# Performance work log

Measured on AMD Instinct MI355X. Metric: run time of the kernel, lower is better.

Reference implementation:

```python
import jax, jax.numpy as jnp
import numpy as np

N = 4096
FIN = 4096
LOC = 16
H1, H2, HEADS = 120, 50, 4
H1_PER = H1 // HEADS
FILM_Z = 32
SSDB_H = 60
N_HEMI = N // 2
NEG_SLOPE = 0.1
GATE_BIAS = -2.0
MASK_FILL = -9e15


def leaky(x):
    return jax.nn.leaky_relu(x, negative_slope=NEG_SLOPE)


def gat(x, mask, W, a_src, a_dst, bias, concat):
    # x: (N, Fin), W: (H, Fin, O), a_src/a_dst: (H, O), mask: (N, N) bool
    wh = jnp.einsum('nf,hfo->hno', x, W)            # (H, N, O)
    f1 = jnp.einsum('hno,ho->hn', wh, a_src)        # (H, N)
    f2 = jnp.einsum('hno,ho->hn', wh, a_dst)        # (H, N)
    e = leaky(f1[:, :, None] + f2[:, None, :])      # (H, N, N)
    e = jnp.where(mask[None], e, MASK_FILL)
    alpha = jax.nn.softmax(e, axis=-1)
    out = jnp.einsum('hij,hjo->hio', alpha, wh)     # (H, N, O)
    if concat:
        h, n, o = out.shape
        out2 = out.transpose(1, 0, 2).reshape(n, h * o)
    else:
        out2 = out.mean(axis=0)
    return out2 + bias


def _uni(k, shape, stdv):
    return jax.random.uniform(k, shape, jnp.float32, -stdv, stdv)


def setup_inputs() -> dict:
    key = jax.random.key(0)
    ks = jax.random.split(key, 30)
    s1 = 1.0 / np.sqrt(H1_PER)
    s2 = 1.0 / np.sqrt(H2)
    inp = {
        'x_fc': jax.random.normal(ks[0], (N, FIN), jnp.float32),
        'adj': jax.random.randint(ks[1], (N, N), 0, 2, jnp.int32),
        'l_loc': jax.random.uniform(ks[2], (N, LOC), jnp.float32),
        # gat1
        'W1': _uni(ks[3], (HEADS, FIN, H1_PER), s1),
        'a1s': _uni(ks[4], (HEADS, H1_PER), s1),
        'a1d': _uni(ks[5], (HEADS, H1_PER), s1),
        'b1': _uni(ks[6], (H1,), s1),
        # gat2
        'W2': _uni(ks[7], (1, H1, H2), s2),
        'a2s': _uni(ks[8], (1, H2), s2),
        'a2d': _uni(ks[9], (1, H2), s2),
        'b2': _uni(ks[10], (H2,), s2),
        # classifier (no bias)
        'Wc': _uni(ks[11], (2, H2), s2),
        # FiLM trunk
        'Wl1': _uni(ks[12], (FILM_Z, LOC), 1.0 / np.sqrt(LOC)),
        'bl1': _uni(ks[13], (FILM_Z,), 1.0 / np.sqrt(LOC)),
        'Wl2': _uni(ks[14], (FILM_Z, FILM_Z), 1.0 / np.sqrt(FILM_Z)),
        'bl2': _uni(ks[15], (FILM_Z,), 1.0 / np.sqrt(FILM_Z)),
        'Wg': _uni(ks[16], (H2, FILM_Z), 1.0 / np.sqrt(FILM_Z)),
        'bg': _uni(ks[17], (H2,), 1.0 / np.sqrt(FILM_Z)),
        'Wb': _uni(ks[18], (H2, FILM_Z), 1.0 / np.sqrt(FILM_Z)),
        'bb': _uni(ks[19], (H2,), 1.0 / np.sqrt(FILM_Z)),
        'Wgate': _uni(ks[20], (1, FILM_Z), 1.0 / np.sqrt(FILM_Z)),
        'bgate': jnp.full((1,), GATE_BIAS, jnp.float32),
        # SSDB hemi
        'Ws1': _uni(ks[21], (SSDB_H, N_HEMI), 1.0 / np.sqrt(N_HEMI)),
        'bs1': _uni(ks[22], (SSDB_H,), 1.0 / np.sqrt(N_HEMI)),
        'Ws2': _uni(ks[23], (1, SSDB_H), 1.0 / np.sqrt(SSDB_H)),
        'bs2': _uni(ks[24], (1,), 1.0 / np.sqrt(SSDB_H)),
    }
    return inp


def reference(x_fc, adj, l_loc, W1, a1s, a1d, b1, W2, a2s, a2d, b2, Wc,
              Wl1, bl1, Wl2, bl2, Wg, bg, Wb, bb, Wgate, bgate,
              Ws1, bs1, Ws2, bs2):
    mask = adj > 0
    h = leaky(gat(x_fc, mask, W1, a1s, a1d, b1, concat=True))    # (N, 120)
    h = leaky(gat(h, mask, W2, a2s, a2d, b2, concat=False))      # (N, 50)
    # FiLM conditioning
    z = leaky(l_loc @ Wl1.T + bl1)
    z = leaky(z @ Wl2.T + bl2)
    gamma = z @ Wg.T + bg                                        # (N, 50)
    beta = z @ Wb.T + bb                                         # (N, 50)
    g = jax.nn.sigmoid(z @ Wgate.T + bgate)                      # (N, 1)
    cov = jnp.clip(l_loc[:, -1], 0.0, 1.0)                       # coverage_power = 1.0
    g = g * cov[:, None]
    h_fused = h + g * (gamma * h + beta)
    logits = leaky(h_fused @ Wc.T)                               # (N, 2)
    # hemisphere SSDB bias
    t = logits.T                                                 # (2, N)
    ipsi = t[:, :N_HEMI]
    contra = t[:, N_HEMI:2 * N_HEMI]
    h_i = leaky(ipsi @ Ws1.T + bs1)                              # (2, 60)
    h_c = leaky(contra @ Ws1.T + bs1)
    b_i = leaky(h_i @ Ws2.T + bs2)                               # (2, 1)
    b_c = leaky(h_c @ Ws2.T + bs2)
    b_mid = 0.5 * (b_i + b_c)                                    # (2, 1)
    bias_nodes = jnp.concatenate([
        jnp.broadcast_to(b_i.T, (N_HEMI, 2)),
        jnp.broadcast_to(b_c.T, (N_HEMI, 2)),
    ], axis=0)                                                   # n_mid = 0
    logits = logits + bias_nodes
    bias_avg = b_mid[:, 0]                                       # (2,)
    return logits, bias_avg
```

## Files before the change

kernel.cpp:

```cpp
#include <hip/hip_runtime.h>

#define NN 4096
#define HEADS 4
#define H1PER 30
#define H1DIM 120
#define H2DIM 50

typedef short short8_t __attribute__((ext_vector_type(8)));
typedef float f32x4 __attribute__((ext_vector_type(4)));

__device__ __forceinline__ float lrelu(float x) { return x > 0.f ? x : 0.1f * x; }

__device__ __forceinline__ unsigned short bfrne(float x) {
  unsigned u = __float_as_uint(x);
  u += 0x7fffu + ((u >> 16) & 1u);
  return (unsigned short)(u >> 16);
}
__device__ __forceinline__ unsigned bfpk_rne(float lo, float hi) {
  return (unsigned)bfrne(lo) | ((unsigned)bfrne(hi) << 16);
}
__device__ __forceinline__ unsigned bfpk(float lo, float hi) {
  unsigned a = (__float_as_uint(lo) + 0x8000u) >> 16;
  unsigned b = (__float_as_uint(hi) + 0x8000u) & 0xffff0000u;
  return a | b;
}
__device__ __forceinline__ float score(float f2v, float f1r, float mr, unsigned bsel, int jj) {
  float f = f1r + f2v;
  float e = fmaxf(f, 0.1f * f);
  float wv = __expf(e - mr);
  return wv * (float)((bsel >> jj) & 1u);
}

__global__ __launch_bounds__(256) void k_bits(const int* __restrict__ adj,
                                              unsigned long long* __restrict__ bits) {
  size_t base = (size_t)blockIdx.x * 1024;
  int t = threadIdx.x;
  int v0 = adj[base + t];
  int v1 = adj[base + 256 + t];
  int v2 = adj[base + 512 + t];
  int v3 = adj[base + 768 + t];
  unsigned long long m0 = __ballot(v0 > 0);
  unsigned long long m1 = __ballot(v1 > 0);
  unsigned long long m2 = __ballot(v2 > 0);
  unsigned long long m3 = __ballot(v3 > 0);
  if ((t & 63) == 0) {
    size_t w = (base + t) >> 6;
    bits[w] = m0;
    bits[w + 4] = m1;
    bits[w + 8] = m2;
    bits[w + 12] = m3;
  }
}

__global__ __launch_bounds__(256) void k_prep(const float* __restrict__ W1,
                                              const float* __restrict__ a1s,
                                              const float* __restrict__ a1d,
                                              unsigned short* __restrict__ w1t) {
  int k = blockIdx.x * 256 + threadIdx.x;
#pragma unroll
  for (int h = 0; h < 4; ++h) {
    const float* wp = W1 + ((size_t)h * 4096 + k) * H1PER;
    float fs = 0.f, fd = 0.f;
#pragma unroll
    for (int oo = 0; oo < H1PER; ++oo) {
      float v = wp[oo];
      w1t[(size_t)(h * 30 + oo) * 4096 + k] = bfrne(v);
      fs += v * a1s[h * H1PER + oo];
      fd += v * a1d[h * H1PER + oo];
    }
    w1t[(size_t)(120 + h) * 4096 + k] = bfrne(fs);
    w1t[(size_t)(124 + h) * 4096 + k] = bfrne(fd);
  }
}

__global__ __launch_bounds__(256) void k_gemm1s(const float* __restrict__ x,
                                                const unsigned short* __restrict__ w1t,
                                                float* __restrict__ part) {
  const int t = threadIdx.x;
  const int lane = t & 63, wave = t >> 6;
  const int m = lane & 15, q = lane >> 4;
  const int i0 = blockIdx.x * 64;
  const int kz = blockIdx.y * 256;
  const float* xp = x + (size_t)(i0 + wave * 16 + m) * 4096 + kz + q * 8;
  const unsigned short* wb = w1t + (size_t)m * 4096 + kz + q * 8;
  f32x4 acc[8];
#pragma unroll
  for (int nt = 0; nt < 8; ++nt) acc[nt] = (f32x4){0.f, 0.f, 0.f, 0.f};
  float4 a0[2], a1[2];
  short8_t Bv[2][8];
  a0[0] = *(const float4*)(xp);
  a1[0] = *(const float4*)(xp + 4);
#pragma unroll
  for (int nt = 0; nt < 8; ++nt) Bv[0][nt] = *(const short8_t*)(wb + (size_t)nt * 16 * 4096);
#pragma unroll
  for (int ks = 0; ks < 8; ++ks) {
    const int cur = ks & 1, nxt = cur ^ 1;
    if (ks < 7) {
      a0[nxt] = *(const float4*)(xp + (ks + 1) * 32);
      a1[nxt] = *(const float4*)(xp + (ks + 1) * 32 + 4);
#pragma unroll
      for (int nt = 0; nt < 8; ++nt)
        Bv[nxt][nt] = *(const short8_t*)(wb + (ks + 1) * 32 + (size_t)nt * 16 * 4096);
    }
    union { short8_t v; unsigned u[4]; } A;
    A.u[0] = bfpk_rne(a0[cur].x, a0[cur].y);
    A.u[1] = bfpk_rne(a0[cur].z, a0[cur].w);
    A.u[2] = bfpk_rne(a1[cur].x, a1[cur].y);
    A.u[3] = bfpk_rne(a1[cur].z, a1[cur].w);
#pragma unroll
    for (int nt = 0; nt < 8; ++nt)
      acc[nt] = __builtin_amdgcn_mfma_f32_16x16x32_bf16(A.v, Bv[cur][nt], acc[nt], 0, 0, 0);
  }
  float* pp = part + ((size_t)blockIdx.y * 4096 + i0 + wave * 16 + q * 4) * 128 + m;
#pragma unroll
  for (int nt = 0; nt < 8; ++nt)
#pragma unroll
    for (int r = 0; r < 4; ++r) pp[r * 128 + nt * 16] = acc[nt][r];
}

__global__ __launch_bounds__(256) void k_f1c(const float* __restrict__ part,
                                             unsigned short* __restrict__ whbt,
                                             float* __restrict__ f1, float* __restrict__ f2) {
  const int t = threadIdx.x;
  const int n = blockIdx.x * 16 + (t >> 4);
  const int og = (t & 15) * 8;
  float s[8] = {0.f, 0.f, 0.f, 0.f, 0.f, 0.f, 0.f, 0.f};
  for (int z = 0; z < 16; ++z) {
    const float* pp = part + ((size_t)z * NN + n) * 128 + og;
    float4 u0 = *(const float4*)pp;
    float4 u1 = *(const float4*)(pp + 4);
    s[0] += u0.x; s[1] += u0.y; s[2] += u0.z; s[3] += u0.w;
    s[4] += u1.x; s[5] += u1.y; s[6] += u1.z; s[7] += u1.w;
  }
  if (og < 120) {
#pragma unroll
    for (int j = 0; j < 8; ++j) {
      int o = og + j;
      int h = o / 30, oo = o - h * 30;
      whbt[(size_t)(h * 32 + oo) * NN + n] = bfrne(s[j]);
    }
  } else {
#pragma unroll
    for (int j = 0; j < 4; ++j) {
      f1[(size_t)j * NN + n] = s[j];
      f2[(size_t)j * NN + n] = s[4 + j];
    }
  }
  if ((t & 15) < 8) {
    int h = (t & 15) >> 1, odd = (t & 15) & 1;
    whbt[(size_t)(h * 32 + 30 + odd) * NN + n] = odd ? 0 : 0x3f80;
  }
}

__global__ __launch_bounds__(256) void k_max(const float* __restrict__ v, float* __restrict__ mx) {
  int t = threadIdx.x;
  const float* row = v + (size_t)blockIdx.x * NN;
  float m = -3.0e38f;
  for (int n = t; n < NN; n += 256) m = fmaxf(m, row[n]);
  for (int off = 32; off > 0; off >>= 1) m = fmaxf(m, __shfl_down(m, off));
  __shared__ float ms[4];
  if ((t & 63) == 0) ms[t >> 6] = m;
  __syncthreads();
  if (t == 0) mx[blockIdx.x] = fmaxf(fmaxf(ms[0], ms[1]), fmaxf(ms[2], ms[3]));
}

__global__ __launch_bounds__(256) void k_att1m(const unsigned short* __restrict__ whbt,
                                               const float* __restrict__ f1, const float* __restrict__ f2,
                                               const float* __restrict__ mx,
                                               const unsigned int* __restrict__ bits32,
                                               float* __restrict__ part) {
  const int h = blockIdx.y, js = blockIdx.z;
  const int t = threadIdx.x;
  const int lane = t & 63, wave = t >> 6;
  const int m = lane & 15, q = lane >> 4;
  const int i0 = blockIdx.x * 64 + wave * 16;
  const int jbase = js * 2048;
  __shared__ float f2s[2048];
  for (int e = t; e < 2048; e += 256) f2s[e] = f2[h * NN + jbase + e];
  __syncthreads();
  const float f1r = f1[h * NN + i0 + m];
  const float fm = f1r + mx[h];
  const float mr = fmaxf(fm, 0.1f * fm);
  const unsigned int* brow = bits32 + (size_t)(i0 + m) * 128 + (jbase >> 5);
  const unsigned short* bb0 = whbt + (size_t)(h * 32 + m) * NN + jbase + q * 8;
  const unsigned short* bb1 = bb0 + 16 * NN;
  const float* fp = f2s + q * 8;
  f32x4 acc0 = {0.f, 0.f, 0.f, 0.f}, acc1 = {0.f, 0.f, 0.f, 0.f};
  for (int step = 0; step < 64; ++step) {
    const int jl = step * 32;
    unsigned bsel = brow[step] >> (q * 8);
    float4 fa = *(const float4*)(fp + jl);
    float4 fb = *(const float4*)(fp + jl + 4);
    float w0 = score(fa.x, f1r, mr, bsel, 0);
    float w1 = score(fa.y, f1r, mr, bsel, 1);
    float w2 = score(fa.z, f1r, mr, bsel, 2);
    float w3 = score(fa.w, f1r, mr, bsel, 3);
    float w4 = score(fb.x, f1r, mr, bsel, 4);
    float w5 = score(fb.y, f1r, mr, bsel, 5);
    float w6 = score(fb.z, f1r, mr, bsel, 6);
    float w7 = score(fb.w, f1r, mr, bsel, 7);
    union { short8_t v; unsigned u[4]; } A;
    A.u[0] = bfpk(w0, w1);
    A.u[1] = bfpk(w2, w3);
    A.u[2] = bfpk(w4, w5);
    A.u[3] = bfpk(w6, w7);
    short8_t b0 = *(const short8_t*)(bb0 + jl);
    short8_t b1 = *(const short8_t*)(bb1 + jl);
    acc0 = __builtin_amdgcn_mfma_f32_16x16x32_bf16(A.v, b0, acc0, 0, 0, 0);
    acc1 = __builtin_amdgcn_mfma_f32_16x16x32_bf16(A.v, b1, acc1, 0, 0, 0);
  }
  float* pp = part + ((size_t)(js * 4 + h) * NN + i0 + q * 4) * 32 + m;
#pragma unroll
  for (int r = 0; r < 4; ++r) {
    pp[r * 32] = acc0[r];
    pp[r * 32 + 16] = acc1[r];
  }
}

__global__ __launch_bounds__(256) void k_h1(const float* __restrict__ part, const float* __restrict__ b1,
                                            float* __restrict__ h1) {
  int t = threadIdx.x;
  int lane = t & 63;
  int p = lane >> 5, o = lane & 31;
  int id = blockIdx.x * 8 + (t >> 6) * 2 + p;
  int h = id >> 12, n = id & 4095;
  const float* p0 = part + ((size_t)h * NN + n) * 32 + o;
  const float* p1 = part + ((size_t)(4 + h) * NN + n) * 32 + o;
  float tot = p0[0] + p1[0];
  float l = __shfl(tot, p * 32 + 30);
  if (o < H1PER) h1[(size_t)n * H1DIM + h * H1PER + o] = lrelu(tot / l + b1[h * H1PER + o]);
}

__global__ __launch_bounds__(256) void k_gemm2(const float* __restrict__ h1, const float* __restrict__ W2,
                                               float* __restrict__ wh2) {
  const int n0 = blockIdx.x * 4;
  const int t = threadIdx.x;
  const int o = t & 63, r = t >> 6;
  __shared__ float hs[4][120];
  for (int e = t; e < 4 * H1DIM; e += 256) hs[e / H1DIM][e % H1DIM] = h1[(size_t)n0 * H1DIM + e];
  __syncthreads();
  if (o < H2DIM) {
    float acc = 0.f;
#pragma unroll 4
    for (int k = 0; k < H1DIM; ++k) acc += hs[r][k] * W2[k * H2DIM + o];
    wh2[(size_t)(n0 + r) * H2DIM + o] = acc;
  }
}

__global__ __launch_bounds__(256) void k_f2l2(const float* __restrict__ wh2, const float* __restrict__ a2s,
                                              const float* __restrict__ a2d, float* __restrict__ f1,
                                              float* __restrict__ f2, unsigned short* __restrict__ whbt) {
  int n = blockIdx.x * 256 + threadIdx.x;
  if (n >= NN) return;
  const float* r = wh2 + (size_t)n * H2DIM;
  unsigned short* wb = whbt + n;
  float accs = 0.f, accd = 0.f;
#pragma unroll
  for (int j = 0; j < H2DIM; ++j) {
    float v = r[j];
    wb[j * NN] = bfrne(v);
    accs += v * a2s[j];
    accd += v * a2d[j];
  }
  wb[50 * NN] = 0x3f80;
#pragma unroll
  for (int j = 51; j < 64; ++j) wb[j * NN] = 0;
  f1[n] = accs;
  f2[n] = accd;
}

__global__ __launch_bounds__(256) void k_att2m(const unsigned short* __restrict__ whbt,
                                               const float* __restrict__ f1, const float* __restrict__ f2,
                                               const float* __restrict__ mx,
                                               const unsigned int* __restrict__ bits32,
                                               float* __restrict__ part) {
  const int js = blockIdx.y;
  const int t = threadIdx.x;
  const int lane = t & 63, wave = t >> 6;
  const int m = lane & 15, q = lane >> 4;
  const int i0 = blockIdx.x * 64 + wave * 16;
  const int jbase = js * 1024;
  __shared__ float f2s[1024];
  for (int e = t; e < 1024; e += 256) f2s[e] = f2[jbase + e];
  __syncthreads();
  const float f1r = f1[i0 + m];
  const float fm = f1r + mx[0];
  const float mr = fmaxf(fm, 0.1f * fm);
  const unsigned int* brow = bits32 + (size_t)(i0 + m) * 128 + (jbase >> 5);
  const unsigned short* bb = whbt + (size_t)m * NN + jbase + q * 8;
  const float* fp = f2s + q * 8;
  f32x4 acc[4];
#pragma unroll
  for (int x = 0; x < 4; ++x) acc[x] = (f32x4){0.f, 0.f, 0.f, 0.f};
  for (int step = 0; step < 32; ++step) {
    const int jl = step * 32;
    unsigned bsel = brow[step] >> (q * 8);
    float4 fa = *(const float4*)(fp + jl);
    float4 fb = *(const float4*)(fp + jl + 4);
    float w0 = score(fa.x, f1r, mr, bsel, 0);
    float w1 = score(fa.y, f1r, mr, bsel, 1);
    float w2 = score(fa.z, f1r, mr, bsel, 2);
    float w3 = score(fa.w, f1r, mr, bsel, 3);
    float w4 = score(fb.x, f1r, mr, bsel, 4);
    float w5 = score(fb.y, f1r, mr, bsel, 5);
    float w6 = score(fb.z, f1r, mr, bsel, 6);
    float w7 = score(fb.w, f1r, mr, bsel, 7);
    union { short8_t v; unsigned u[4]; } A;
    A.u[0] = bfpk(w0, w1);
    A.u[1] = bfpk(w2, w3);
    A.u[2] = bfpk(w4, w5);
    A.u[3] = bfpk(w6, w7);
#pragma unroll
    for (int tile = 0; tile < 4; ++tile) {
      short8_t b = *(const short8_t*)(bb + (size_t)tile * 16 * NN + jl);
      acc[tile] = __builtin_amdgcn_mfma_f32_16x16x32_bf16(A.v, b, acc[tile], 0, 0, 0);
    }
  }
  float* pp = part + ((size_t)js * NN + i0 + q * 4) * 64 + m;
#pragma unroll
  for (int tile = 0; tile < 4; ++tile)
#pragma unroll
    for (int r = 0; r < 4; ++r) pp[r * 64 + tile * 16] = acc[tile][r];
}

__global__ __launch_bounds__(64) void k_h2(const float* __restrict__ part, const float* __restrict__ b2,
                                           float* __restrict__ h2) {
  int n = blockIdx.x;
  int o = threadIdx.x;
  const float* p = part + (size_t)n * 64 + o;
  float tot = p[0] + p[NN * 64] + p[2 * NN * 64] + p[3 * NN * 64];
  float l = __shfl(tot, 50);
  if (o < H2DIM) h2[(size_t)n * H2DIM + o] = lrelu(tot / l + b2[o]);
}

__global__ __launch_bounds__(256) void k_film(const float* __restrict__ l_loc, const float* __restrict__ h2,
                                              const float* __restrict__ Wl1, const float* __restrict__ bl1,
                                              const float* __restrict__ Wl2, const float* __restrict__ bl2,
                                              const float* __restrict__ Wg, const float* __restrict__ bg,
                                              const float* __restrict__ Wb, const float* __restrict__ bb,
                                              const float* __restrict__ Wgate, const float* __restrict__ bgate,
                                              const float* __restrict__ Wc, float* __restrict__ logits) {
  int n = blockIdx.x * 4 + (threadIdx.x >> 6);
  int lane = threadIdx.x & 63;
  int r32 = lane & 31;
  float locv = l_loc[n * 16 + (lane & 15)];
  float cov = __shfl(locv, 15);
  cov = fminf(fmaxf(cov, 0.f), 1.f);
  float a1v = bl1[r32];
#pragma unroll
  for (int j = 0; j < 16; ++j) a1v += Wl1[r32 * 16 + j] * __shfl(locv, j);
  float z1 = lrelu(a1v);
  float a2v = bl2[r32];
#pragma unroll
  for (int j = 0; j < 32; ++j) a2v += Wl2[r32 * 32 + j] * __shfl(z1, j);
  float z2 = lrelu(a2v);
  float gs = bgate[0];
  float gam, bet;
  {
    int o = lane < H2DIM ? lane : 0;
    gam = bg[o];
    bet = bb[o];
#pragma unroll
    for (int j = 0; j < 32; ++j) {
      float zj = __shfl(z2, j);
      gs += Wgate[j] * zj;
      gam += Wg[o * 32 + j] * zj;
      bet += Wb[o * 32 + j] * zj;
    }
  }
  float g = cov / (1.f + __expf(-gs));
  int o = lane < H2DIM ? lane : 0;
  float hv = h2[(size_t)n * H2DIM + o];
  float hf = hv + g * (gam * hv + bet);
  float p0 = lane < H2DIM ? hf * Wc[o] : 0.f;
  float p1 = lane < H2DIM ? hf * Wc[H2DIM + o] : 0.f;
  for (int off = 32; off > 0; off >>= 1) {
    p0 += __shfl_down(p0, off);
    p1 += __shfl_down(p1, off);
  }
  if (lane == 0) {
    logits[n * 2 + 0] = lrelu(p0);
    logits[n * 2 + 1] = lrelu(p1);
  }
}

__global__ __launch_bounds__(64) void k_ssdb1(const float* __restrict__ logits, const float* __restrict__ Ws1,
                                              float* __restrict__ hsum) {
  int combo = blockIdx.y;
  int hemi = combo >> 1, c = combo & 1;
  int k = threadIdx.x;
  if (k >= 60) return;
  int nbase = blockIdx.x * 256;
  const float* wrow = Ws1 + (size_t)k * 2048 + nbase;
  const float* lcol = logits + (size_t)(hemi * 2048 + nbase) * 2 + c;
  float part = 0.f;
  for (int q = 0; q < 256; ++q) part += wrow[q] * lcol[2 * q];
  atomicAdd(&hsum[combo * 60 + k], part);
}

__global__ __launch_bounds__(256) void k_ssdb2(const float* __restrict__ hsum, const float* __restrict__ bs1,
                                               const float* __restrict__ Ws2, const float* __restrict__ bs2,
                                               float* __restrict__ B) {
  int t = threadIdx.x;
  int combo = t >> 6, k = t & 63;
  float part = 0.f;
  if (k < 60) part = lrelu(hsum[combo * 60 + k] + bs1[k]) * Ws2[k];
  for (int off = 32; off > 0; off >>= 1) part += __shfl_down(part, off);
  if (k == 0) B[combo] = lrelu(part + bs2[0]);
}

__global__ __launch_bounds__(256) void k_final(const float* __restrict__ logits, const float* __restrict__ B,
                                               float* __restrict__ out) {
  int id = blockIdx.x * 256 + threadIdx.x;
  if (id < 2 * NN) {
    int n = id >> 1, c = id & 1;
    out[id] = logits[id] + B[(n < 2048 ? 0 : 2) + c];
  } else if (id < 2 * NN + 2) {
    int c = id - 2 * NN;
    out[id] = 0.5f * (B[c] + B[2 + c]);
  }
}

#define OFF_BITS 0
#define OFF_W1T 524288
#define OFF_GP 786432
#define OFF_A1P 786432
#define OFF_A2P 1835008
#define OFF_H1 2883584
#define OFF_WH2 3375104
#define OFF_WH2BT 3579904
#define OFF_F12 3710976
#define OFF_F22 3715072
#define OFF_MX2 3719168
#define OFF_H2 3719232
#define OFF_LOG 3924032
#define OFF_HSUM 3932224
#define OFF_B 3932480
#define OFF_WH1BT 9175040
#define OFF_F1A 9437184
#define OFF_F2A 9453568
#define OFF_MX1 9469952

extern "C" void kernel_launch(void* const* d_in, const int* in_sizes, int n_in,
                              void* d_out, int out_size, void* d_ws, size_t ws_size,
                              hipStream_t stream) {
  const float* x_fc  = (const float*)d_in[0];
  const int*   adj   = (const int*)d_in[1];
  const float* l_loc = (const float*)d_in[2];
  const float* W1    = (const float*)d_in[3];
  const float* a1s   = (const float*)d_in[4];
  const float* a1d   = (const float*)d_in[5];
  const float* b1    = (const float*)d_in[6];
  const float* W2    = (const float*)d_in[7];
  const float* a2s   = (const float*)d_in[8];
  const float* a2d   = (const float*)d_in[9];
  const float* b2    = (const float*)d_in[10];
  const float* Wc    = (const float*)d_in[11];
  const float* Wl1   = (const float*)d_in[12];
  const float* bl1   = (const float*)d_in[13];
  const float* Wl2   = (const float*)d_in[14];
  const float* bl2   = (const float*)d_in[15];
  const float* Wg    = (const float*)d_in[16];
  const float* bg    = (const float*)d_in[17];
  const float* Wb    = (const float*)d_in[18];
  const float* bb    = (const float*)d_in[19];
  const float* Wgate = (const float*)d_in[20];
  const float* bgate = (const float*)d_in[21];
  const float* Ws1   = (const float*)d_in[22];
  const float* bs1   = (const float*)d_in[23];
  const float* Ws2   = (const float*)d_in[24];
  const float* bs2   = (const float*)d_in[25];
  float* out = (float*)d_out;
  float* w = (float*)d_ws;
  unsigned long long* bits = (unsigned long long*)(w + OFF_BITS);
  const unsigned int* bits32 = (const unsigned int*)bits;
  unsigned short* wh1bt = (unsigned short*)(w + OFF_WH1BT);
  unsigned short* wh2bt = (unsigned short*)(w + OFF_WH2BT);
  unsigned short* w1t = (unsigned short*)(w + OFF_W1T);

  k_bits<<<NN * NN / 1024, 256, 0, stream>>>(adj, bits);
  k_prep<<<16, 256, 0, stream>>>(W1, a1s, a1d, w1t);
  k_gemm1s<<<dim3(64, 16), 256, 0, stream>>>(x_fc, w1t, w + OFF_GP);
  k_f1c<<<256, 256, 0, stream>>>(w + OFF_GP, wh1bt, w + OFF_F1A, w + OFF_F2A);
  k_max<<<HEADS, 256, 0, stream>>>(w + OFF_F2A, w + OFF_MX1);
  k_att1m<<<dim3(64, HEADS, 2), 256, 0, stream>>>(wh1bt, w + OFF_F1A, w + OFF_F2A,
                                                  w + OFF_MX1, bits32, w + OFF_A1P);
  k_h1<<<2048, 256, 0, stream>>>(w + OFF_A1P, b1, w + OFF_H1);
  k_gemm2<<<NN / 4, 256, 0, stream>>>(w + OFF_H1, W2, w + OFF_WH2);
  k_f2l2<<<NN / 256, 256, 0, stream>>>(w + OFF_WH2, a2s, a2d, w + OFF_F12, w + OFF_F22, wh2bt);
  k_max<<<1, 256, 0, stream>>>(w + OFF_F22, w + OFF_MX2);
  k_att2m<<<dim3(64, 4), 256, 0, stream>>>(wh2bt, w + OFF_F12, w + OFF_F22,
                                           w + OFF_MX2, bits32, w + OFF_A2P);
  k_h2<<<NN, 64, 0, stream>>>(w + OFF_A2P, b2, w + OFF_H2);
  k_film<<<NN / 4, 256, 0, stream>>>(l_loc, w + OFF_H2, Wl1, bl1, Wl2, bl2, Wg, bg, Wb, bb,
                                     Wgate, bgate, Wc, w + OFF_LOG);
  hipMemsetAsync(w + OFF_HSUM, 0, 240 * sizeof(float), stream);
  k_ssdb1<<<dim3(8, 4), 64, 0, stream>>>(w + OFF_LOG, Ws1, w + OFF_HSUM);
  k_ssdb2<<<1, 256, 0, stream>>>(w + OFF_HSUM, bs1, Ws2, bs2, w + OFF_B);
  k_final<<<(2 * NN + 2 + 255) / 256, 256, 0, stream>>>(w + OFF_LOG, w + OFF_B, out);
}
```

Baseline: 365.6 us.

## Stage x tiles in LDS via global_load_lds and retile split-K GEMM

Rewrites the first GEMM to copy x tiles into swizzled shared memory with direct global-to-LDS loads instead of per-thread register prefetch. The block tile changes from 64 rows by 256 K to 32 rows by 512 K, with waves split across output column groups, which halves the split-K partial count that k_f1c must reduce. B fragments are now loaded straight from global memory inside the loop without double buffering, and each iteration adds block barriers, so load latency may be less hidden.

```diff
diff --git a/kernel.cpp b/kernel.cpp
--- a/kernel.cpp
+++ b/kernel.cpp
@@ -30,6 +30,10 @@
   float wv = __expf(e - mr);
   return wv * (float)((bsel >> jj) & 1u);
 }
+
+#define GL16(g, l)                                                                        \
+  __builtin_amdgcn_global_load_lds((const __attribute__((address_space(1))) unsigned int*)(g), \
+                                   (__attribute__((address_space(3))) unsigned int*)(l), 16, 0, 0)
 
 __global__ __launch_bounds__(256) void k_bits(const int* __restrict__ adj,
                                               unsigned long long* __restrict__ bits) {
@@ -79,41 +83,51 @@
   const int t = threadIdx.x;
   const int lane = t & 63, wave = t >> 6;
   const int m = lane & 15, q = lane >> 4;
-  const int i0 = blockIdx.x * 64;
-  const int kz = blockIdx.y * 256;
-  const float* xp = x + (size_t)(i0 + wave * 16 + m) * 4096 + kz + q * 8;
-  const unsigned short* wb = w1t + (size_t)m * 4096 + kz + q * 8;
-  f32x4 acc[8];
-#pragma unroll
-  for (int nt = 0; nt < 8; ++nt) acc[nt] = (f32x4){0.f, 0.f, 0.f, 0.f};
-  float4 a0[2], a1[2];
-  short8_t Bv[2][8];
-  a0[0] = *(const float4*)(xp);
-  a1[0] = *(const float4*)(xp + 4);
-#pragma unroll
-  for (int nt = 0; nt < 8; ++nt) Bv[0][nt] = *(const short8_t*)(wb + (size_t)nt * 16 * 4096);
-#pragma unroll
-  for (int ks = 0; ks < 8; ++ks) {
-    const int cur = ks & 1, nxt = cur ^ 1;
-    if (ks < 7) {
-      a0[nxt] = *(const float4*)(xp + (ks + 1) * 32);
-      a1[nxt] = *(const float4*)(xp + (ks + 1) * 32 + 4);
-#pragma unroll
-      for (int nt = 0; nt < 8; ++nt)
-        Bv[nxt][nt] = *(const short8_t*)(wb + (ks + 1) * 32 + (size_t)nt * 16 * 4096);
+  const int i0 = blockIdx.x * 32;
+  const int kz = blockIdx.y * 512;
+  __shared__ float xs[32 * 64];
+  const int r0 = (wave & 1) * 16;
+  const int ntg0 = (wave >> 1) * 4;
+  const int srow0 = wave * 8 + q;
+  const int srow1 = srow0 + 4;
+  const int sc0 = m ^ (srow0 & 7);
+  const int sc1 = m ^ (srow1 & 7);
+  const float* gx0 = x + (size_t)(i0 + srow0) * 4096 + kz + sc0 * 4;
+  const float* gx1 = x + (size_t)(i0 + srow1) * 4096 + kz + sc1 * 4;
+  float* ls0 = &xs[srow0 * 64 + m * 4];
+  float* ls1 = &xs[srow1 * 64 + m * 4];
+  const int arow = r0 + m;
+  const int asw = (m & 7);
+  f32x4 acc[4];
+#pragma unroll
+  for (int nt = 0; nt < 4; ++nt) acc[nt] = (f32x4){0.f, 0.f, 0.f, 0.f};
+  for (int it = 0; it < 8; ++it) {
+    const int kc = it * 64;
+    GL16(gx0 + kc, ls0);
+    GL16(gx1 + kc, ls1);
+    __syncthreads();
+#pragma unroll
+    for (int ks2 = 0; ks2 < 2; ++ks2) {
+      const int c0 = ks2 * 8 + q * 2;
+      float4 a0 = *(const float4*)&xs[arow * 64 + ((c0 ^ asw) * 4)];
+      float4 a1 = *(const float4*)&xs[arow * 64 + (((c0 + 1) ^ asw) * 4)];
+      union { short8_t v; unsigned u[4]; } A;
+      A.u[0] = bfpk_rne(a0.x, a0.y);
+      A.u[1] = bfpk_rne(a0.z, a0.w);
+      A.u[2] = bfpk_rne(a1.x, a1.y);
+      A.u[3] = bfpk_rne(a1.z, a1.w);
+      const unsigned short* wp = w1t + (size_t)m * 4096 + kz + kc + ks2 * 32 + q * 8;
+#pragma unroll
+      for (int nt = 0; nt < 4; ++nt) {
+        short8_t B = *(const short8_t*)(wp + (size_t)(ntg0 + nt) * 16 * 4096);
+        acc[nt] = __builtin_amdgcn_mfma_f32_16x16x32_bf16(A.v, B, acc[nt], 0, 0, 0);
+      }
     }
-    union { short8_t v; unsigned u[4]; } A;
-    A.u[0] = bfpk_rne(a0[cur].x, a0[cur].y);
-    A.u[1] = bfpk_rne(a0[cur].z, a0[cur].w);
-    A.u[2] = bfpk_rne(a1[cur].x, a1[cur].y);
-    A.u[3] = bfpk_rne(a1[cur].z, a1[cur].w);
-#pragma unroll
-    for (int nt = 0; nt < 8; ++nt)
-      acc[nt] = __builtin_amdgcn_mfma_f32_16x16x32_bf16(A.v, Bv[cur][nt], acc[nt], 0, 0, 0);
-  }
-  float* pp = part + ((size_t)blockIdx.y * 4096 + i0 + wave * 16 + q * 4) * 128 + m;
-#pragma unroll
-  for (int nt = 0; nt < 8; ++nt)
+    __syncthreads();
+  }
+  float* pp = part + ((size_t)blockIdx.y * 4096 + i0 + r0 + q * 4) * 128 + ntg0 * 16 + m;
+#pragma unroll
+  for (int nt = 0; nt < 4; ++nt)
 #pragma unroll
     for (int r = 0; r < 4; ++r) pp[r * 128 + nt * 16] = acc[nt][r];
 }
@@ -125,7 +139,7 @@
   const int n = blockIdx.x * 16 + (t >> 4);
   const int og = (t & 15) * 8;
   float s[8] = {0.f, 0.f, 0.f, 0.f, 0.f, 0.f, 0.f, 0.f};
-  for (int z = 0; z < 16; ++z) {
+  for (int z = 0; z < 8; ++z) {
     const float* pp = part + ((size_t)z * NN + n) * 128 + og;
     float4 u0 = *(const float4*)pp;
     float4 u1 = *(const float4*)(pp + 4);
@@ -480,7 +494,7 @@
 
   k_bits<<<NN * NN / 1024, 256, 0, stream>>>(adj, bits);
   k_prep<<<16, 256, 0, stream>>>(W1, a1s, a1d, w1t);
-  k_gemm1s<<<dim3(64, 16), 256, 0, stream>>>(x_fc, w1t, w + OFF_GP);
+  k_gemm1s<<<dim3(128, 8), 256, 0, stream>>>(x_fc, w1t, w + OFF_GP);
   k_f1c<<<256, 256, 0, stream>>>(w + OFF_GP, wh1bt, w + OFF_F1A, w + OFF_F2A);
   k_max<<<HEADS, 256, 0, stream>>>(w + OFF_F2A, w + OFF_MX1);
   k_att1m<<<dim3(64, HEADS, 2), 256, 0, stream>>>(wh1bt, w + OFF_F1A, w + OFF_F2A,
```

Measured after the change: 359.2 us. Within noise of the previous version (-1.7%).
